# Performance work log

Hardware: AMD Instinct MI355X
Metric: run time of the kernel (lower is better)

The kernel has to match this reference:

```python
import jax, jax.numpy as jnp
import numpy as np

N_NODES = 100000
N_EDGES = 1600000
D_FEAT = 64
LATENT = 64
N_CLASSES = 16
NEG_SLOPE = 0.01  # flax nn.leaky_relu default negative_slope


def setup_inputs() -> dict:
    key = jax.random.key(0)
    ks = jax.random.split(key, 5)
    nodes = jax.random.normal(ks[0], (N_NODES, D_FEAT), dtype=jnp.float32)
    senders = jax.random.randint(ks[1], (N_EDGES,), 0, N_NODES)
    receivers = jax.random.randint(ks[2], (N_EDGES,), 0, N_NODES)
    # learned params (flax Dense: y = x @ kernel + bias)
    W0 = jax.random.normal(ks[3], (D_FEAT, LATENT), dtype=jnp.float32) / jnp.sqrt(D_FEAT)
    b0 = jnp.zeros((LATENT,), jnp.float32)
    W1 = jax.random.normal(ks[4], (LATENT, N_CLASSES), dtype=jnp.float32) / jnp.sqrt(LATENT)
    b1 = jnp.zeros((N_CLASSES,), jnp.float32)
    return {"nodes": nodes, "senders": senders, "receivers": receivers,
            "W0": W0, "b0": b0, "W1": W1, "b1": b1}


def _gcn_forward(nodes, W0, b0, W1, b1, senders, receivers):
    n = nodes.shape[0]
    ones = jnp.ones_like(senders, dtype=nodes.dtype)
    deg_s = jax.ops.segment_sum(ones, senders, n)    # out-degree of each node as sender
    deg_r = jax.ops.segment_sum(ones, receivers, n)  # in-degree of each node as receiver

    # Layer 1: GraphConvolution(Dense(latent), symmetric_normalization=True)
    h = nodes @ W0 + b0                                                  # [N, latent]
    h = h * jax.lax.rsqrt(jnp.maximum(deg_s, 1.0))[:, None]
    h = jax.ops.segment_sum(h[senders], receivers, n)                    # gather-scatter over edges
    h = h * jax.lax.rsqrt(jnp.maximum(deg_r, 1.0))[:, None]
    h = jnp.where(h >= 0, h, NEG_SLOPE * h)                              # leaky_relu

    # Layer 2: GraphConvolution(Dense(classes)+sigmoid, symmetric_normalization=False)
    z = jax.nn.sigmoid(h @ W1 + b1)                                      # [N, classes]
    out = jax.ops.segment_sum(z[senders], receivers, n)                  # unnormalized aggregation
    return out


def reference(nodes, senders, receivers, W0, b0, W1, b1):
    return _gcn_forward(nodes, W0, b0, W1, b1, senders, receivers)
```

## Files before the change

kernel.cpp:

```cpp
#include <hip/hip_runtime.h>
#include <hip/hip_bf16.h>

#define NN 100000
#define NE 1600000
#define D 64
#define C 16
#define NEG_SLOPE 0.01f
#define MCAP 64

#define NRG 8
#define RGW 12500
#define RWORDS 3125
#define NSR 64
#define EPSR 25000
#define B_RH (NSR * NRG)

#define NRANGE 8
#define RW 12544
#define WPR 3136
#define NSLICE 64
#define EPS 25000
#define B_HS (NRANGE * NSLICE)

#define B_GEMM 6250

typedef unsigned int u32;
typedef unsigned short u16;

__device__ __forceinline__ float bf2f(u32 u) { return __uint_as_float(u << 16); }
__device__ __forceinline__ u16 f2bf(float f) {
    __hip_bfloat16 b = __float2bfloat16(f);
    return *reinterpret_cast<u16*>(&b);
}

__global__ __launch_bounds__(256) void kA(
        const int* __restrict__ senders, const int* __restrict__ receivers,
        const float* __restrict__ nodes, const float* __restrict__ W0,
        const float* __restrict__ b0,
        u32* __restrict__ part_r, u32* __restrict__ part_s, u16* __restrict__ h) {
    __shared__ u32 smh[WPR];
    int bid = blockIdx.x, t = threadIdx.x;

    if (bid < B_RH) {
        int slice = bid >> 3, range = bid & 7;
        int lo = range * RGW;
        for (int i = t; i < RWORDS; i += 256) smh[i] = 0u;
        __syncthreads();
        const int* __restrict__ rp = receivers + slice * EPSR;
        for (int i = t; i < EPSR; i += 256) {
            int rl = rp[i] - lo;
            if ((u32)rl < (u32)RGW)
                atomicAdd(&smh[rl >> 2], 1u << ((rl & 3) * 8));
        }
        __syncthreads();
        u32* __restrict__ dst = part_r + ((size_t)slice * NRG + range) * RWORDS;
        for (int i = t; i < RWORDS; i += 256) dst[i] = smh[i];
    } else if (bid < B_RH + B_HS) {
        int hb = bid - B_RH;
        int rr = hb & 7, sl = hb >> 3;
        int lo = rr * RW;
        for (int i = t; i < WPR; i += 256) smh[i] = 0u;
        __syncthreads();
        const int* __restrict__ sp = senders + sl * EPS;
        for (int i = t; i < EPS; i += 256) {
            int local = sp[i] - lo;
            if ((u32)local < (u32)RW)
                atomicAdd(&smh[local >> 2], 1u << ((local & 3) * 8));
        }
        __syncthreads();
        u32* __restrict__ dst = part_s + (size_t)hb * WPR;
        for (int i = t; i < WPR; i += 256) dst[i] = smh[i];
    } else {
        int wv = (bid - B_RH - B_HS) * 4 + (t >> 6);
        int lane = t & 63;
        int nsub = lane >> 4, q = lane & 15;
        int node = wv * 4 + nsub;
        const float* __restrict__ row = nodes + (size_t)node * D;
        float4 acc = ((const float4*)b0)[q];
#pragma unroll 16
        for (int k = 0; k < D; ++k) {
            float rk = row[k];
            float4 w4 = ((const float4*)(W0 + k * D))[q];
            acc.x = fmaf(rk, w4.x, acc.x);
            acc.y = fmaf(rk, w4.y, acc.y);
            acc.z = fmaf(rk, w4.z, acc.z);
            acc.w = fmaf(rk, w4.w, acc.w);
        }
        uint2 pk;
        pk.x = (u32)f2bf(acc.x) | ((u32)f2bf(acc.y) << 16);
        pk.y = (u32)f2bf(acc.z) | ((u32)f2bf(acc.w) << 16);
        *(uint2*)(h + (size_t)node * D + q * 4) = pk;
    }
}

__global__ __launch_bounds__(256) void kSc(u32* __restrict__ part_r,
                                           const u32* __restrict__ part_s,
                                           int* __restrict__ cnt_r,
                                           float* __restrict__ rnorm_s) {
    int bid = blockIdx.x, t = threadIdx.x;
    if (bid < 98) {
        int tid = bid * 256 + t;
        if (tid < NRG * RWORDS) {
            int range = tid / RWORDS, w = tid - range * RWORDS;
            u32* __restrict__ base = part_r + (size_t)range * RWORDS + w;
            u32 s0 = 0, s1 = 0, s2 = 0, s3 = 0;
            for (int sl = 0; sl < NSR; ++sl) {
                u32* p = base + (size_t)sl * (NRG * RWORDS);
                u32 v = *p;
                *p = s0 | (s1 << 8) | (s2 << 16) | (s3 << 24);
                s0 += v & 0xffu;
                s1 += (v >> 8) & 0xffu;
                s2 += (v >> 16) & 0xffu;
                s3 += (v >> 24) & 0xffu;
            }
            int node = range * RGW + w * 4;
            int4 cv; cv.x = (int)s0; cv.y = (int)s1; cv.z = (int)s2; cv.w = (int)s3;
            *(int4*)(cnt_r + node) = cv;
        }
    } else {
        int tid = (bid - 98) * 256 + t;
        if (tid < NRANGE * WPR) {
            int rr = tid / WPR;
            int w = tid - rr * WPR;
            const u32* __restrict__ p = part_s + (size_t)rr * WPR + w;
            u32 acc0 = 0, acc1 = 0;
#pragma unroll 8
            for (int sl = 0; sl < NSLICE; ++sl) {
                u32 v = p[(size_t)(sl * 8) * WPR];
                acc0 += v & 0x00FF00FFu;
                acc1 += (v >> 8) & 0x00FF00FFu;
            }
            int node = rr * RW + w * 4;
            u32 c0 = acc0 & 0xFFFFu, c1 = acc1 & 0xFFFFu, c2 = acc0 >> 16, c3 = acc1 >> 16;
            if (node + 3 < NN) {
                float4 o;
                o.x = rsqrtf((float)(c0 > 1u ? c0 : 1u));
                o.y = rsqrtf((float)(c1 > 1u ? c1 : 1u));
                o.z = rsqrtf((float)(c2 > 1u ? c2 : 1u));
                o.w = rsqrtf((float)(c3 > 1u ? c3 : 1u));
                *(float4*)(rnorm_s + node) = o;
            } else {
                u32 cc[4] = {c0, c1, c2, c3};
                for (int k = 0; k < 4; ++k)
                    if (node + k < NN)
                        rnorm_s[node + k] = rsqrtf((float)(cc[k] > 1u ? cc[k] : 1u));
            }
        }
    }
}

__global__ __launch_bounds__(256) void kF(
        const int* __restrict__ senders, const int* __restrict__ receivers,
        const u32* __restrict__ part_r,
        int* __restrict__ bucket) {
    __shared__ u32 smh[RWORDS];
    int bid = blockIdx.x, t = threadIdx.x;
    int slice = bid >> 3, range = bid & 7;
    int lo = range * RGW;
    const u32* __restrict__ pre = part_r + ((size_t)slice * NRG + range) * RWORDS;
    for (int i = t; i < RWORDS; i += 256) smh[i] = pre[i];
    __syncthreads();
    int e0 = slice * EPSR;
    for (int i = t; i < EPSR; i += 256) {
        int e = e0 + i;
        int rl = receivers[e] - lo;
        if ((u32)rl < (u32)RGW) {
            int s = senders[e];
            int w = rl >> 2, sh = (rl & 3) * 8;
            u32 old = atomicAdd(&smh[w], 1u << sh);
            int slot = (int)((old >> sh) & 0xffu);
            if (slot < MCAP)
                bucket[(lo + rl) * MCAP + slot] = s;
        }
    }
}

__global__ __launch_bounds__(256) void kB(
        const int* __restrict__ cnt_r, const int* __restrict__ bucket,
        const float* __restrict__ rnorm_s, const u16* __restrict__ h,
        const float* __restrict__ W1, const float* __restrict__ b1,
        u16* __restrict__ z) {
    __shared__ float sm[4][64];
    int wid = threadIdx.x >> 6, lane = threadIdx.x & 63;
    int node = blockIdx.x * 4 + wid;
    int deg = cnt_r[node];
    if (deg > MCAP) deg = MCAP;
    const int* __restrict__ row = bucket + node * MCAP;

    int my = 0; float rq = 0.f;
    if (lane < deg) {
        my = row[lane];
        rq = rnorm_s[my];
    }
    int qtr = lane >> 4, ql = lane & 15;
    float a0 = 0.f, a1 = 0.f, a2 = 0.f, a3 = 0.f;
    for (int j = 0; j < deg; j += 4) {
        int ei = j + qtr;
        int src = __shfl(my, ei, 64);
        float rs = __shfl(rq, ei, 64);
        uint2 w2 = *(const uint2*)(h + (size_t)src * D + ql * 4);
        if (ei < deg) {
            a0 = fmaf(rs, bf2f(w2.x & 0xffffu), a0);
            a1 = fmaf(rs, bf2f(w2.x >> 16),     a1);
            a2 = fmaf(rs, bf2f(w2.y & 0xffffu), a2);
            a3 = fmaf(rs, bf2f(w2.y >> 16),     a3);
        }
    }
    a0 += __shfl_xor(a0, 16, 64); a0 += __shfl_xor(a0, 32, 64);
    a1 += __shfl_xor(a1, 16, 64); a1 += __shfl_xor(a1, 32, 64);
    a2 += __shfl_xor(a2, 16, 64); a2 += __shfl_xor(a2, 32, 64);
    a3 += __shfl_xor(a3, 16, 64); a3 += __shfl_xor(a3, 32, 64);
    if (qtr == 0) {
        float rn = rsqrtf((float)(deg > 1 ? deg : 1));
        float v0 = a0 * rn; v0 = (v0 >= 0.f) ? v0 : NEG_SLOPE * v0;
        float v1 = a1 * rn; v1 = (v1 >= 0.f) ? v1 : NEG_SLOPE * v1;
        float v2 = a2 * rn; v2 = (v2 >= 0.f) ? v2 : NEG_SLOPE * v2;
        float v3 = a3 * rn; v3 = (v3 >= 0.f) ? v3 : NEG_SLOPE * v3;
        sm[wid][ql * 4 + 0] = v0;
        sm[wid][ql * 4 + 1] = v1;
        sm[wid][ql * 4 + 2] = v2;
        sm[wid][ql * 4 + 3] = v3;
    }
    __syncthreads();

    int c = lane & 15, q = lane >> 4;
    float p = 0.f;
#pragma unroll
    for (int i = 0; i < 16; ++i)
        p = fmaf(sm[wid][q * 16 + i], W1[(q * 16 + i) * C + c], p);
    p += __shfl_xor(p, 16, 64);
    p += __shfl_xor(p, 32, 64);
    if (lane < 16) {
        float zc = 1.f / (1.f + expf(-(p + b1[c])));
        z[(size_t)node * C + c] = f2bf(zc);
    }
}

__global__ __launch_bounds__(256) void kC(
        const int* __restrict__ cnt_r, const int* __restrict__ bucket,
        const u16* __restrict__ z, float* __restrict__ out) {
    int idx = blockIdx.x * 256 + threadIdx.x;
    int node = idx >> 6;
    int lane = threadIdx.x & 63;
    int deg = cnt_r[node];
    if (deg > MCAP) deg = MCAP;
    const int* __restrict__ row = bucket + node * MCAP;

    int my = (lane < deg) ? row[lane] : 0;
    int g = lane >> 2, p = lane & 3;
    float a0 = 0.f, a1 = 0.f, a2 = 0.f, a3 = 0.f;
    for (int j = 0; j < deg; j += 16) {
        int ei = j + g;
        int src = __shfl(my, ei, 64);
        uint2 w2 = *(const uint2*)(z + (size_t)src * C + p * 4);
        if (ei < deg) {
            a0 += bf2f(w2.x & 0xffffu);
            a1 += bf2f(w2.x >> 16);
            a2 += bf2f(w2.y & 0xffffu);
            a3 += bf2f(w2.y >> 16);
        }
    }
    a0 += __shfl_xor(a0, 4, 64); a0 += __shfl_xor(a0, 8, 64);
    a0 += __shfl_xor(a0, 16, 64); a0 += __shfl_xor(a0, 32, 64);
    a1 += __shfl_xor(a1, 4, 64); a1 += __shfl_xor(a1, 8, 64);
    a1 += __shfl_xor(a1, 16, 64); a1 += __shfl_xor(a1, 32, 64);
    a2 += __shfl_xor(a2, 4, 64); a2 += __shfl_xor(a2, 8, 64);
    a2 += __shfl_xor(a2, 16, 64); a2 += __shfl_xor(a2, 32, 64);
    a3 += __shfl_xor(a3, 4, 64); a3 += __shfl_xor(a3, 8, 64);
    a3 += __shfl_xor(a3, 16, 64); a3 += __shfl_xor(a3, 32, 64);
    if (lane < 4) {
        float4 o; o.x = a0; o.y = a1; o.z = a2; o.w = a3;
        *(float4*)(out + (size_t)node * C + p * 4) = o;
    }
}

extern "C" void kernel_launch(void* const* d_in, const int* in_sizes, int n_in,
                              void* d_out, int out_size, void* d_ws, size_t ws_size,
                              hipStream_t stream) {
    const float* nodes     = (const float*)d_in[0];
    const int*   senders   = (const int*)d_in[1];
    const int*   receivers = (const int*)d_in[2];
    const float* W0        = (const float*)d_in[3];
    const float* b0        = (const float*)d_in[4];
    const float* W1        = (const float*)d_in[5];
    const float* b1        = (const float*)d_in[6];
    float* out = (float*)d_out;

    char* wsb = (char*)d_ws;
    u32*   part_r  = (u32*)wsb;
    u32*   part_s  = (u32*)(wsb + 6400000);
    int*   cnt_r   = (int*)(wsb + 12822528);
    float* rnorm_s = (float*)(wsb + 13222528);
    int*   bucket  = (int*)(wsb + 13622528);
    u16*   h       = (u16*)(wsb + 39222528);
    u16*   z       = (u16*)(wsb + 52022528);

    kA<<<B_RH + B_HS + B_GEMM, 256, 0, stream>>>(senders, receivers, nodes, W0, b0,
                                                 part_r, part_s, h);
    kSc<<<196, 256, 0, stream>>>(part_r, part_s, cnt_r, rnorm_s);
    kF<<<B_RH, 256, 0, stream>>>(senders, receivers, part_r, bucket);
    kB<<<25000, 256, 0, stream>>>(cnt_r, bucket, rnorm_s, h, W1, b1, z);
    kC<<<25000, 256, 0, stream>>>(cnt_r, bucket, z, out);
}
```

Before: 310.1 us.

## Vectorize edge index loads, pack four nodes per wave in kC, drop kB barrier

Result: faster. 278.2 us (-10.3%).

```diff
diff --git a/kernel.cpp b/kernel.cpp
--- a/kernel.cpp
+++ b/kernel.cpp
@@ -47,10 +47,13 @@
         for (int i = t; i < RWORDS; i += 256) smh[i] = 0u;
         __syncthreads();
         const int* __restrict__ rp = receivers + slice * EPSR;
-        for (int i = t; i < EPSR; i += 256) {
-            int rl = rp[i] - lo;
-            if ((u32)rl < (u32)RGW)
-                atomicAdd(&smh[rl >> 2], 1u << ((rl & 3) * 8));
+        for (int i = 4 * t; i < EPSR; i += 1024) {
+            int4 v = *(const int4*)(rp + i);
+            int r0 = v.x - lo, r1 = v.y - lo, r2 = v.z - lo, r3 = v.w - lo;
+            if ((u32)r0 < (u32)RGW) atomicAdd(&smh[r0 >> 2], 1u << ((r0 & 3) * 8));
+            if ((u32)r1 < (u32)RGW) atomicAdd(&smh[r1 >> 2], 1u << ((r1 & 3) * 8));
+            if ((u32)r2 < (u32)RGW) atomicAdd(&smh[r2 >> 2], 1u << ((r2 & 3) * 8));
+            if ((u32)r3 < (u32)RGW) atomicAdd(&smh[r3 >> 2], 1u << ((r3 & 3) * 8));
         }
         __syncthreads();
         u32* __restrict__ dst = part_r + ((size_t)slice * NRG + range) * RWORDS;
@@ -62,10 +65,13 @@
         for (int i = t; i < WPR; i += 256) smh[i] = 0u;
         __syncthreads();
         const int* __restrict__ sp = senders + sl * EPS;
-        for (int i = t; i < EPS; i += 256) {
-            int local = sp[i] - lo;
-            if ((u32)local < (u32)RW)
-                atomicAdd(&smh[local >> 2], 1u << ((local & 3) * 8));
+        for (int i = 4 * t; i < EPS; i += 1024) {
+            int4 v = *(const int4*)(sp + i);
+            int s0 = v.x - lo, s1 = v.y - lo, s2 = v.z - lo, s3 = v.w - lo;
+            if ((u32)s0 < (u32)RW) atomicAdd(&smh[s0 >> 2], 1u << ((s0 & 3) * 8));
+            if ((u32)s1 < (u32)RW) atomicAdd(&smh[s1 >> 2], 1u << ((s1 & 3) * 8));
+            if ((u32)s2 < (u32)RW) atomicAdd(&smh[s2 >> 2], 1u << ((s2 & 3) * 8));
+            if ((u32)s3 < (u32)RW) atomicAdd(&smh[s3 >> 2], 1u << ((s3 & 3) * 8));
         }
         __syncthreads();
         u32* __restrict__ dst = part_s + (size_t)hb * WPR;
@@ -160,17 +166,38 @@
     const u32* __restrict__ pre = part_r + ((size_t)slice * NRG + range) * RWORDS;
     for (int i = t; i < RWORDS; i += 256) smh[i] = pre[i];
     __syncthreads();
-    int e0 = slice * EPSR;
-    for (int i = t; i < EPSR; i += 256) {
-        int e = e0 + i;
-        int rl = receivers[e] - lo;
+    const int* __restrict__ rp = receivers + slice * EPSR;
+    const int* __restrict__ sp = senders + slice * EPSR;
+    for (int i = 4 * t; i < EPSR; i += 1024) {
+        int4 rv = *(const int4*)(rp + i);
+        int rl;
+        rl = rv.x - lo;
         if ((u32)rl < (u32)RGW) {
-            int s = senders[e];
             int w = rl >> 2, sh = (rl & 3) * 8;
             u32 old = atomicAdd(&smh[w], 1u << sh);
             int slot = (int)((old >> sh) & 0xffu);
-            if (slot < MCAP)
-                bucket[(lo + rl) * MCAP + slot] = s;
+            if (slot < MCAP) bucket[(lo + rl) * MCAP + slot] = sp[i];
+        }
+        rl = rv.y - lo;
+        if ((u32)rl < (u32)RGW) {
+            int w = rl >> 2, sh = (rl & 3) * 8;
+            u32 old = atomicAdd(&smh[w], 1u << sh);
+            int slot = (int)((old >> sh) & 0xffu);
+            if (slot < MCAP) bucket[(lo + rl) * MCAP + slot] = sp[i + 1];
+        }
+        rl = rv.z - lo;
+        if ((u32)rl < (u32)RGW) {
+            int w = rl >> 2, sh = (rl & 3) * 8;
+            u32 old = atomicAdd(&smh[w], 1u << sh);
+            int slot = (int)((old >> sh) & 0xffu);
+            if (slot < MCAP) bucket[(lo + rl) * MCAP + slot] = sp[i + 2];
+        }
+        rl = rv.w - lo;
+        if ((u32)rl < (u32)RGW) {
+            int w = rl >> 2, sh = (rl & 3) * 8;
+            u32 old = atomicAdd(&smh[w], 1u << sh);
+            int slot = (int)((old >> sh) & 0xffu);
+            if (slot < MCAP) bucket[(lo + rl) * MCAP + slot] = sp[i + 3];
         }
     }
 }
@@ -221,7 +248,7 @@
         sm[wid][ql * 4 + 2] = v2;
         sm[wid][ql * 4 + 3] = v3;
     }
-    __syncthreads();
+    asm volatile("s_waitcnt lgkmcnt(0)" ::: "memory");
 
     int c = lane & 15, q = lane >> 4;
     float p = 0.f;
@@ -239,36 +266,36 @@
 __global__ __launch_bounds__(256) void kC(
         const int* __restrict__ cnt_r, const int* __restrict__ bucket,
         const u16* __restrict__ z, float* __restrict__ out) {
-    int idx = blockIdx.x * 256 + threadIdx.x;
-    int node = idx >> 6;
-    int lane = threadIdx.x & 63;
+    int t = threadIdx.x;
+    int lane = t & 63;
+    int qtr = lane >> 4, ql = lane & 15;
+    int node = blockIdx.x * 16 + (t >> 6) * 4 + qtr;
     int deg = cnt_r[node];
     if (deg > MCAP) deg = MCAP;
     const int* __restrict__ row = bucket + node * MCAP;
 
-    int my = (lane < deg) ? row[lane] : 0;
-    int g = lane >> 2, p = lane & 3;
+    int g2 = ql >> 2, p = ql & 3;
     float a0 = 0.f, a1 = 0.f, a2 = 0.f, a3 = 0.f;
-    for (int j = 0; j < deg; j += 16) {
-        int ei = j + g;
-        int src = __shfl(my, ei, 64);
-        uint2 w2 = *(const uint2*)(z + (size_t)src * C + p * 4);
-        if (ei < deg) {
-            a0 += bf2f(w2.x & 0xffffu);
-            a1 += bf2f(w2.x >> 16);
-            a2 += bf2f(w2.y & 0xffffu);
-            a3 += bf2f(w2.y >> 16);
+    for (int base = 0; base < deg; base += 16) {
+        int nb = deg - base; if (nb > 16) nb = 16;
+        int my = (ql < nb) ? row[base + ql] : 0;
+        for (int j = 0; j < nb; j += 4) {
+            int ei = j + g2;
+            int src = __shfl(my, (lane & 48) | ei, 64);
+            uint2 w2 = *(const uint2*)(z + (size_t)src * C + p * 4);
+            if (ei < nb) {
+                a0 += bf2f(w2.x & 0xffffu);
+                a1 += bf2f(w2.x >> 16);
+                a2 += bf2f(w2.y & 0xffffu);
+                a3 += bf2f(w2.y >> 16);
+            }
         }
     }
     a0 += __shfl_xor(a0, 4, 64); a0 += __shfl_xor(a0, 8, 64);
-    a0 += __shfl_xor(a0, 16, 64); a0 += __shfl_xor(a0, 32, 64);
     a1 += __shfl_xor(a1, 4, 64); a1 += __shfl_xor(a1, 8, 64);
-    a1 += __shfl_xor(a1, 16, 64); a1 += __shfl_xor(a1, 32, 64);
     a2 += __shfl_xor(a2, 4, 64); a2 += __shfl_xor(a2, 8, 64);
-    a2 += __shfl_xor(a2, 16, 64); a2 += __shfl_xor(a2, 32, 64);
     a3 += __shfl_xor(a3, 4, 64); a3 += __shfl_xor(a3, 8, 64);
-    a3 += __shfl_xor(a3, 16, 64); a3 += __shfl_xor(a3, 32, 64);
-    if (lane < 4) {
+    if (g2 == 0) {
         float4 o; o.x = a0; o.y = a1; o.z = a2; o.w = a3;
         *(float4*)(out + (size_t)node * C + p * 4) = o;
     }
@@ -300,5 +327,5 @@
     kSc<<<196, 256, 0, stream>>>(part_r, part_s, cnt_r, rnorm_s);
     kF<<<B_RH, 256, 0, stream>>>(senders, receivers, part_r, bucket);
     kB<<<25000, 256, 0, stream>>>(cnt_r, bucket, rnorm_s, h, W1, b1, z);
-    kC<<<25000, 256, 0, stream>>>(cnt_r, bucket, z, out);
-}
+    kC<<<6250, 256, 0, stream>>>(cnt_r, bucket, z, out);
+}
```
